# Optimization experiments

Measured on AMD Instinct MI355X. Metric: run time of the kernel, lower is better.

Reference implementation:

```python
import math
import jax, jax.numpy as jnp
import numpy as np

RMS_EPS = 1.1920929e-07  # torch.finfo(float32).eps used by F.rms_norm default

def _rms_norm(x):
    return x * jax.lax.rsqrt(jnp.mean(jnp.square(x), axis=-1, keepdims=True) + RMS_EPS)

def _rope(x, cos, sin):
    # x: [B,T,H,D]; cos/sin: [T, D//2]
    d = x.shape[-1] // 2
    x1, x2 = x[..., :d], x[..., d:]
    c = cos[None, :, None, :]
    s = sin[None, :, None, :]
    return jnp.concatenate([x1 * c + x2 * s, -x1 * s + x2 * c], axis=-1).astype(x.dtype)

def setup_inputs():
    key = jax.random.key(0)
    ks = jax.random.split(key, 8)
    B, T, C, H, D = 2, 2048, 2048, 16, 128
    x = jax.random.normal(ks[0], (B, T, C), dtype=jnp.float32)
    # real RoPE tables for [T, D//2]
    half = D // 2
    inv_freq = 1.0 / (10000.0 ** (np.arange(half, dtype=np.float32) / half))
    ang = np.outer(np.arange(T, dtype=np.float32), inv_freq)
    cos = jnp.asarray(np.cos(ang), dtype=jnp.float32)
    sin = jnp.asarray(np.sin(ang), dtype=jnp.float32)
    s = 0.02
    Wq = jax.random.normal(ks[1], (C, H * D), dtype=jnp.float32) * s
    Wk = jax.random.normal(ks[2], (C, H * D), dtype=jnp.float32) * s
    Wv = jax.random.normal(ks[3], (C, H * D), dtype=jnp.float32) * s
    Wo = jax.random.normal(ks[4], (C, C), dtype=jnp.float32) * s
    fgate_w = jax.random.normal(ks[5], (C, H), dtype=jnp.float32) * s
    fgate_b = jnp.zeros((H,), dtype=jnp.float32)
    weight_lambda = jax.random.normal(ks[6], (C, H), dtype=jnp.float32) * s
    return dict(x=x, cos=cos, sin=sin, Wq=Wq, Wk=Wk, Wv=Wv, Wo=Wo,
                fgate_w=fgate_w, fgate_b=fgate_b, weight_lambda=weight_lambda,
                window_size=1024)

def reference(x, cos, sin, Wq, Wk, Wv, Wo, fgate_w, fgate_b, weight_lambda, window_size):
    B, T, C = x.shape
    H = fgate_w.shape[1]
    D = Wq.shape[1] // H
    sm_scale = 1.0 / math.sqrt(D)
    # QKV projections (bias=False)
    q = (x @ Wq).reshape(B, T, H, D)
    k = (x @ Wk).reshape(B, T, H, D)
    v = (x @ Wv).reshape(B, T, H, D)
    # RoPE then parameter-free RMSNorm on q,k
    q = _rms_norm(_rope(q, cos, sin))
    k = _rms_norm(_rope(k, cos, sin))
    # [B,H,T,D]
    q = q.transpose(0, 2, 1, 3)
    k = k.transpose(0, 2, 1, 3)
    v = v.transpose(0, 2, 1, 3)
    # forgetting gate: log f_t per (B,H,T)
    lam = jax.nn.elu((x @ weight_lambda).astype(jnp.float32)) + 1.0          # [B,T,H]
    logit = (x @ fgate_w + fgate_b) * lam                                    # [B,T,H]
    log_fgate = (jax.nn.log_sigmoid(logit) / (lam + 0.001)).transpose(0, 2, 1)  # [B,H,T]
    cumF = jnp.cumsum(log_fgate, axis=-1)                                    # [B,H,T]
    # forgetting flash attention, dense reference: bias_ij = cumF_i - cumF_j
    scores = jnp.einsum('bhqd,bhkd->bhqk', q.astype(jnp.float32), k.astype(jnp.float32)) * sm_scale
    scores = scores + cumF[..., :, None] - cumF[..., None, :]
    i = jnp.arange(T)[:, None]
    j = jnp.arange(T)[None, :]
    allowed = (j <= i) & (i - j < window_size)  # causal + sliding window
    scores = jnp.where(allowed, scores, -jnp.inf)
    attn = jax.nn.softmax(scores, axis=-1)
    y = jnp.einsum('bhqk,bhkd->bhqd', attn, v.astype(jnp.float32)).astype(x.dtype)
    y = y.transpose(0, 2, 1, 3).reshape(B, T, C)
    return y @ Wo
```

## Files before the change

### kernel.cpp

```cpp
#include <hip/hip_runtime.h>
#include <hip/hip_bf16.h>
#include <stdint.h>

#define T_SEQ 2048
#define CDIM  2048
#define NHEAD 16
#define DHEAD 128
#define BT    4096
#define BHT   32
#define NQKV  6144

typedef __bf16 bf16x8_t __attribute__((ext_vector_type(8)));
typedef float  f32x4_t  __attribute__((ext_vector_type(4)));
typedef unsigned short u16x8_t __attribute__((ext_vector_type(8)));
typedef unsigned short u16x4_t __attribute__((ext_vector_type(4)));

__device__ __forceinline__ unsigned short f2bf(float f){
  unsigned int u = __float_as_uint(f);
  u += 0x7fffu + ((u >> 16) & 1u);
  return (unsigned short)(u >> 16);
}
__device__ __forceinline__ float bf2f(unsigned short h){
  return __uint_as_float(((unsigned int)h) << 16);
}
__device__ __forceinline__ unsigned ldsaddr(const void* p){
  return (unsigned)(size_t)(const __attribute__((address_space(3))) void*)p;
}
__device__ __forceinline__ u16x4_t tr16(unsigned a){
  u16x4_t r;
  asm volatile("ds_read_b64_tr_b16 %0, %1" : "=v"(r) : "v"(a));
  return r;
}

__global__ __launch_bounds__(256) void transpose_cast(const float* __restrict__ W,
                                                      unsigned short* __restrict__ Wt){
  __shared__ float tile[32][33];
  int n0 = blockIdx.x*32, k0 = blockIdx.y*32;
  int tx = threadIdx.x, ty = threadIdx.y;
  #pragma unroll
  for (int i=0;i<32;i+=8)
    tile[ty+i][tx] = W[(size_t)(k0+ty+i)*CDIM + n0 + tx];
  __syncthreads();
  #pragma unroll
  for (int i=0;i<32;i+=8)
    Wt[(size_t)(n0+ty+i)*CDIM + k0 + tx] = f2bf(tile[tx][ty+i]);
}

__global__ __launch_bounds__(256) void build_wgt(const float* __restrict__ fgw,
                                                 const float* __restrict__ wlam,
                                                 float* __restrict__ WgT){
  int idx = blockIdx.x*256 + threadIdx.x;
  int c = idx >> 11, k = idx & 2047;
  const float* W = (c < 16) ? fgw : wlam;
  WgT[idx] = W[k*16 + (c & 15)];
}


#define V3_SYNC() do{ __builtin_amdgcn_sched_barrier(0); \
  __builtin_amdgcn_s_barrier(); \
  asm volatile("s_waitcnt lgkmcnt(0)" ::: "memory"); \
  __builtin_amdgcn_sched_barrier(0); }while(0)

#define V3_TAIL() do{ asm volatile("s_waitcnt vmcnt(3)" ::: "memory"); \
  __builtin_amdgcn_sched_barrier(0); \
  __builtin_amdgcn_s_barrier(); }while(0)

#define V3_MFMA() do{ __builtin_amdgcn_s_setprio(1); \
  _Pragma("unroll") for (int mi=0;mi<4;mi++) \
  _Pragma("unroll") for (int ni=0;ni<4;ni++) \
    acc[mi][ni] = __builtin_amdgcn_mfma_f32_16x16x32_bf16(af[mi], bfr[ni], acc[mi][ni],0,0,0); \
  __builtin_amdgcn_s_setprio(0); }while(0)

#define V3_PHASE(BUF, TIDX) do{ \
  readA(BUF); readB(BUF); \
  { int ts_ = (TIDX)+2; if (ts_ > ntm1) ts_ = ntm1; stage(((BUF)+2)%3, ts_); } \
  V3_SYNC(); V3_MFMA(); V3_TAIL(); }while(0)

template<int MODE>
__global__ __launch_bounds__(512, 2) void gemm_v3(const unsigned short* __restrict__ A,
                                                  const unsigned short* __restrict__ Bt,
                                                  void* __restrict__ Cout,
                                                  int M, int N, int K){
  extern __shared__ unsigned short lds[];
  const int nx = N >> 8;
  const int Mt = M >> 7;
  const int bid = blockIdx.x;
  const int c8 = bid & 7, w = bid >> 3;
  const int mh = Mt >> 1;
  const int mt = (c8 & 1)*mh + (w % mh);
  const int ntc = (c8 >> 1)*(nx >> 2) + (w / mh);
  const int m0 = mt << 7, n0 = ntc << 8;
  const int tid = threadIdx.x, lane = tid & 63, wv = tid >> 6;
  const int wm = wv >> 2, wn = wv & 3;
  const int g = lane >> 4, qi = lane & 15;
  const int ntm1 = (K >> 5) - 1;

  f32x4_t acc[4][4] = {};
  bf16x8_t af[4], bfr[4];

  int goffA, goffB[2];
  { int s = tid; int row = s >> 2; int lg = (s & 3) ^ ((row >> 1) & 3);
    goffA = row*K + lg*8; }
  #pragma unroll
  for (int j=0;j<2;j++){
    int s = j*512 + tid;
    int row = s >> 2;
    int lg = (s & 3) ^ ((row >> 1) & 3);
    goffB[j] = row*K + lg*8;
  }

  auto stage = [&](int buf, int kt){
    const unsigned short* srcA = A + (size_t)m0*K + kt*32;
    const unsigned short* srcB = Bt + (size_t)n0*K + kt*32;
    unsigned short* base = lds + buf*12288;
    __builtin_amdgcn_global_load_lds(
        (const __attribute__((address_space(1))) void*)(srcA + goffA),
        (__attribute__((address_space(3))) void*)(base + tid*8), 16, 0, 0);
    #pragma unroll
    for (int j=0;j<2;j++)
      __builtin_amdgcn_global_load_lds(
        (const __attribute__((address_space(1))) void*)(srcB + goffB[j]),
        (__attribute__((address_space(3))) void*)(base + 4096 + (j*512 + tid)*8), 16, 0, 0);
  };
  auto readA = [&](int buf){
    const unsigned short* base = lds + buf*12288;
    #pragma unroll
    for (int mi=0;mi<4;mi++){
      int row = wm*64 + mi*16 + qi;
      int gs = g ^ ((row >> 1) & 3);
      af[mi] = *reinterpret_cast<const bf16x8_t*>(base + (row*4 + gs)*8);
    }
  };
  auto readB = [&](int buf){
    const unsigned short* base = lds + buf*12288 + 4096;
    #pragma unroll
    for (int ni=0;ni<4;ni++){
      int row = wn*64 + ni*16 + qi;
      int gs = g ^ ((row >> 1) & 3);
      bfr[ni] = *reinterpret_cast<const bf16x8_t*>(base + (row*4 + gs)*8);
    }
  };

  stage(0,0); stage(1,1);
  asm volatile("s_waitcnt vmcnt(3)" ::: "memory");
  __builtin_amdgcn_sched_barrier(0);
  __builtin_amdgcn_s_barrier();

  for (int it=0; it<21; ++it){
    const int t3 = it*3;
    V3_PHASE(0, t3+0);
    V3_PHASE(1, t3+1);
    V3_PHASE(2, t3+2);
  }
  V3_PHASE(0, 63);
  asm volatile("s_waitcnt vmcnt(0)" ::: "memory");

  #pragma unroll
  for (int mi=0;mi<4;mi++){
    #pragma unroll
    for (int ni=0;ni<4;ni++){
      #pragma unroll
      for (int r=0;r<4;r++){
        int mm = m0 + wm*64 + mi*16 + 4*g + r;
        int nn = n0 + wn*64 + ni*16 + qi;
        float v = acc[mi][ni][r];
        if (MODE == 2){
          ((float*)Cout)[(size_t)mm*N + nn] = v;
        } else {
          int bb2 = mm >> 11, t = mm & (T_SEQ-1);
          int which = nn >> 11;
          int hh = (nn >> 7) & 15, d = nn & (DHEAD-1);
          ((unsigned short*)Cout)[(size_t)which*8388608 +
              (((size_t)bb2*NHEAD + hh)*T_SEQ + t)*DHEAD + d] = f2bf(v);
        }
      }
    }
  }
}

#define GROWS 4
__global__ __launch_bounds__(256) void gates_kernel(const float* __restrict__ x,
    const float* __restrict__ WgT, const float* __restrict__ fgb,
    float* __restrict__ lfg, unsigned short* __restrict__ xb){
  __shared__ float xs[GROWS*2048];
  __shared__ float part[GROWS*32*8];
  const int r0 = blockIdx.x*GROWS;
  const int tid = threadIdx.x;
  const float* xp = x + (size_t)r0*CDIM;
  #pragma unroll
  for (int i=0;i<GROWS*2048/(256*4); i++){
    int e = (i*256+tid)*4;
    *(float4*)(xs+e) = *(const float4*)(xp+e);
  }
  __syncthreads();
  #pragma unroll
  for (int i=0;i<GROWS*2048/(256*8); i++){
    int e = (i*256+tid)*8;
    u16x8_t ob;
    #pragma unroll
    for (int j=0;j<8;j++) ob[j] = f2bf(xs[e+j]);
    *reinterpret_cast<u16x8_t*>(xb + (size_t)r0*CDIM + e) = ob;
  }
  const int c = tid & 31, kseg = tid >> 5;
  const float* wp = WgT + c*2048 + kseg*256;
  const float* xq = xs + kseg*256;
  f32x4_t acc[GROWS] = {};
  for (int kk=0; kk<64; kk++){
    f32x4_t wv = *(const f32x4_t*)(wp + kk*4);
    #pragma unroll
    for (int r=0;r<GROWS;r++){
      f32x4_t xv = *(const f32x4_t*)(xq + r*2048 + kk*4);
      acc[r] += xv*wv;
    }
  }
  #pragma unroll
  for (int r=0;r<GROWS;r++)
    part[(r*32 + c)*8 + kseg] = acc[r][0]+acc[r][1]+acc[r][2]+acc[r][3];
  __syncthreads();
  if (tid < GROWS*32){
    const int r = tid >> 5, c2 = tid & 31;
    const float* pp = part + (r*32+c2)*8;
    float s = pp[0]+pp[1]+pp[2]+pp[3]+pp[4]+pp[5]+pp[6]+pp[7];
    float other = __shfl_xor(s, 16, 64);
    if (c2 < 16){
      float df = s, dl = other;
      float lam = (dl > 0.f) ? (dl + 1.f) : __expf(dl);
      float logit = (df + fgb[c2]) * lam;
      float ls = fminf(logit, 0.f) - log1pf(__expf(-fabsf(logit)));
      float lf = ls / (lam + 0.001f);
      int row = r0 + r;
      int b = row >> 11, t = row & (T_SEQ-1);
      lfg[((size_t)b*NHEAD + c2)*T_SEQ + t] = lf;
    }
  }
}

__global__ __launch_bounds__(256) void cumsum_kernel(const float* __restrict__ lfg,
                                                     float* __restrict__ cumF){
  __shared__ float sums[256];
  const int bh = blockIdx.x;
  const float* in = lfg + (size_t)bh*T_SEQ;
  float* out = cumF + (size_t)bh*T_SEQ;
  const int tid = threadIdx.x;
  float4 a = *(const float4*)(in + tid*8);
  float4 b = *(const float4*)(in + tid*8 + 4);
  float v[8] = {a.x,a.y,a.z,a.w,b.x,b.y,b.z,b.w};
  float run = 0.f;
  #pragma unroll
  for (int e=0;e<8;e++) run += v[e];
  sums[tid] = run;
  __syncthreads();
  for (int off=1; off<256; off<<=1){
    float y = (tid >= off) ? sums[tid-off] : 0.f;
    __syncthreads();
    sums[tid] += y;
    __syncthreads();
  }
  float acc = sums[tid] - run;
  float o[8];
  #pragma unroll
  for (int e=0;e<8;e++){ acc += v[e]; o[e] = acc; }
  *(float4*)(out + tid*8)     = make_float4(o[0],o[1],o[2],o[3]);
  *(float4*)(out + tid*8 + 4) = make_float4(o[4],o[5],o[6],o[7]);
}

__global__ __launch_bounds__(256) void rope_rms(unsigned short* __restrict__ QK,
    const float* __restrict__ cosT, const float* __restrict__ sinT){
  const int tid = threadIdx.x, lane = tid & 63, wv = tid >> 6;
  const int idx2 = blockIdx.x*4 + wv;
  const int which = idx2 >> 16;
  const int row = idx2 & 65535;
  const int t = row & (T_SEQ-1);
  unsigned short* xp = QK + (size_t)which*8388608 + (size_t)row*DHEAD;
  float x1 = bf2f(xp[lane]);
  float x2 = bf2f(xp[lane+64]);
  float c = cosT[t*64 + lane];
  float s = sinT[t*64 + lane];
  float o1 = x1*c + x2*s;
  float o2 = x2*c - x1*s;
  float ss = o1*o1 + o2*o2;
  #pragma unroll
  for (int off=1; off<64; off<<=1) ss += __shfl_xor(ss, off, 64);
  float scale = rsqrtf(ss*(1.f/128.f) + 1.1920929e-07f);
  xp[lane]    = f2bf(o1*scale);
  xp[lane+64] = f2bf(o2*scale);
}

__global__ __launch_bounds__(256, 2) void attn_kernel(const unsigned short* __restrict__ Qh,
    const unsigned short* __restrict__ Kh, const unsigned short* __restrict__ Vh,
    const float* __restrict__ cumF, unsigned short* __restrict__ Y,
    const int* __restrict__ winp){
  __shared__ unsigned short smem[32768];
  const int dlin = blockIdx.y*16 + blockIdx.x;
  const int c8 = dlin & 7, klin = dlin >> 3;
  const int bh = c8 + 8*(klin >> 4);
  const int q0b = (klin & 15)*128;
  const int b = bh >> 4, h = bh & 15;
  const int tid = threadIdx.x, lane = tid & 63, wv = tid >> 6;
  const int g = lane >> 4, qi = lane & 15;
  const int win = *winp;
  const unsigned short* Qp = Qh + (size_t)bh*T_SEQ*DHEAD;
  const unsigned short* Kp = Kh + (size_t)bh*T_SEQ*DHEAD;
  const unsigned short* Vp = Vh + (size_t)bh*T_SEQ*DHEAD;
  const float* cF = cumF + (size_t)bh*T_SEQ;
  const int q0w = q0b + wv*32;
  bf16x8_t qf[2][4];
  float cFq[2];
  #pragma unroll
  for (int qb=0;qb<2;qb++){
    cFq[qb] = cF[q0w + qb*16 + qi];
    #pragma unroll
    for (int dt=0;dt<4;dt++)
      qf[qb][dt] = *reinterpret_cast<const bf16x8_t*>(Qp + (size_t)(q0w + qb*16 + qi)*DHEAD + dt*32 + g*8);
  }
  f32x4_t ot[2][8] = {};
  float mrun[2] = {-1e30f, -1e30f}, lrun[2] = {0.f, 0.f};
  const float sm_scale = 0.08838834764831845f;
  int kbeg = q0b - win + 1; if (kbeg < 0) kbeg = 0; kbeg &= ~63;
  const int nt = (q0b + 128 - kbeg) >> 6;

  auto stage = [&](int bi, int k0s){
    unsigned short* Kd = smem + bi*8192;
    unsigned short* Vd = smem + 16384 + bi*8192;
    #pragma unroll
    for (int jj=0;jj<4;jj++){
      int t = (wv*4+jj)*64 + lane;
      int r = t>>4, cc = t&15;
      __builtin_amdgcn_global_load_lds(
        (const __attribute__((address_space(1))) void*)(Kp + (size_t)(k0s+r)*DHEAD + ((cc ^ (r&7))*8)),
        (__attribute__((address_space(3))) void*)(Kd + t*8), 16, 0, 0);
      int dd = t>>7, kq = (t>>3)&15, rr = (t>>1)&3, hb = t&1;
      __builtin_amdgcn_global_load_lds(
        (const __attribute__((address_space(1))) void*)(Vp + (size_t)(k0s + kq*4 + rr)*DHEAD + dd*16 + hb*8),
        (__attribute__((address_space(3))) void*)(Vd + t*8), 16, 0, 0);
    }
  };

  stage(0, kbeg);
  for (int it=0; it<nt; ++it){
    const int k0 = kbeg + it*64;
    const int cur = it & 1;
    __syncthreads();
    if (it+1 < nt) stage(cur^1, k0+64);
    if (k0 <= q0w+31 && (k0 + 63) >= (q0w - win + 1)){
      const unsigned short* Kc = smem + cur*8192;
      f32x4_t s[2][4] = {};
      __builtin_amdgcn_s_setprio(1);
      #pragma unroll
      for (int dt=0;dt<4;dt++){
        bf16x8_t kf[4];
        #pragma unroll
        for (int kb=0;kb<4;kb++){
          int row = kb*16 + qi;
          kf[kb] = *reinterpret_cast<const bf16x8_t*>(Kc + row*128 + (((dt*4+g) ^ (row&7))*8));
        }
        #pragma unroll
        for (int kb=0;kb<4;kb++){
          s[0][kb] = __builtin_amdgcn_mfma_f32_16x16x32_bf16(kf[kb], qf[0][dt], s[0][kb], 0,0,0);
          s[1][kb] = __builtin_amdgcn_mfma_f32_16x16x32_bf16(kf[kb], qf[1][dt], s[1][kb], 0,0,0);
        }
      }
      __builtin_amdgcn_s_setprio(0);
      float4 cb[4];
      #pragma unroll
      for (int kb=0;kb<4;kb++) cb[kb] = *(const float4*)(cF + k0 + kb*16 + 4*g);
      u16x8_t pb[2][2];
      #pragma unroll
      for (int qb=0;qb<2;qb++){
        const int qg = q0w + qb*16 + qi;
        float p[16], tmax = -INFINITY;
        #pragma unroll
        for (int kb=0;kb<4;kb++){
          #pragma unroll
          for (int r=0;r<4;r++){
            int key = k0 + kb*16 + 4*g + r;
            float sv = fmaf(s[qb][kb][r], sm_scale, cFq[qb] - ((const float*)&cb[kb])[r]);
            bool ok = (key <= qg) && (qg - key < win);
            p[kb*4+r] = ok ? sv : -INFINITY;
            tmax = fmaxf(tmax, p[kb*4+r]);
          }
        }
        tmax = fmaxf(tmax, __shfl_xor(tmax, 16, 64));
        tmax = fmaxf(tmax, __shfl_xor(tmax, 32, 64));
        float mnew = fmaxf(mrun[qb], tmax);
        float alpha = __expf(mrun[qb] - mnew);
        float tsum = 0.f;
        #pragma unroll
        for (int i2=0;i2<16;i2++){ p[i2] = __expf(p[i2] - mnew); tsum += p[i2]; }
        tsum += __shfl_xor(tsum, 16, 64);
        tsum += __shfl_xor(tsum, 32, 64);
        lrun[qb] = lrun[qb]*alpha + tsum;
        mrun[qb] = mnew;
        #pragma unroll
        for (int dt=0;dt<8;dt++) ot[qb][dt] *= alpha;
        #pragma unroll
        for (int cc=0;cc<2;cc++){
          #pragma unroll
          for (int e=0;e<8;e++)
            pb[qb][cc][e] = f2bf(p[(2*cc + (e>>2))*4 + (e&3)]);
        }
      }
      unsigned vbase = ldsaddr(smem + 16384 + cur*8192) + lane*8;
      #pragma unroll
      for (int cc=0;cc<2;cc++){
        u16x4_t vlo[8], vhi[8];
        #pragma unroll
        for (int dt=0;dt<8;dt++){
          vlo[dt] = tr16(vbase + (unsigned)((dt*16 + 8*cc)*128));
          vhi[dt] = tr16(vbase + (unsigned)((dt*16 + 8*cc + 4)*128));
        }
        asm volatile("s_waitcnt lgkmcnt(0)");
        __builtin_amdgcn_sched_barrier(0);
        __builtin_amdgcn_s_setprio(1);
        #pragma unroll
        for (int dt=0;dt<8;dt++){
          u16x8_t vv = __builtin_shufflevector(vlo[dt], vhi[dt], 0,1,2,3,4,5,6,7);
          bf16x8_t vf = *reinterpret_cast<bf16x8_t*>(&vv);
          ot[0][dt] = __builtin_amdgcn_mfma_f32_16x16x32_bf16(vf, *reinterpret_cast<bf16x8_t*>(&pb[0][cc]), ot[0][dt], 0,0,0);
          ot[1][dt] = __builtin_amdgcn_mfma_f32_16x16x32_bf16(vf, *reinterpret_cast<bf16x8_t*>(&pb[1][cc]), ot[1][dt], 0,0,0);
        }
        __builtin_amdgcn_s_setprio(0);
      }
    }
  }
  __syncthreads();
  float invl[2] = {1.f/lrun[0], 1.f/lrun[1]};
  #pragma unroll
  for (int qb=0;qb<2;qb++){
    int qlocal = wv*32 + qb*16 + qi;
    #pragma unroll
    for (int dt=0;dt<8;dt++){
      int d8 = dt*2 + (g>>1);
      u16x4_t w;
      #pragma unroll
      for (int r=0;r<4;r++) w[r] = f2bf(ot[qb][dt][r]*invl[qb]);
      *reinterpret_cast<u16x4_t*>(smem + qlocal*128 + ((d8 ^ (qlocal&7))*8) + 4*(g&1)) = w;
    }
  }
  __syncthreads();
  #pragma unroll
  for (int i=0;i<8;i++){
    int t = i*256 + tid;
    int row = t>>4, cc = t&15;
    u16x8_t v = *reinterpret_cast<const u16x8_t*>(smem + row*128 + ((cc ^ (row&7))*8));
    *reinterpret_cast<u16x8_t*>(Y + ((size_t)b*T_SEQ + q0b + row)*CDIM + h*DHEAD + cc*8) = v;
  }
}

extern "C" void kernel_launch(void* const* d_in, const int* in_sizes, int n_in,
                              void* d_out, int out_size, void* d_ws, size_t ws_size,
                              hipStream_t stream){
  const float* x    = (const float*)d_in[0];
  const float* cosT = (const float*)d_in[1];
  const float* sinT = (const float*)d_in[2];
  const float* Wq   = (const float*)d_in[3];
  const float* Wk   = (const float*)d_in[4];
  const float* Wv   = (const float*)d_in[5];
  const float* Wo   = (const float*)d_in[6];
  const float* fgw  = (const float*)d_in[7];
  const float* fgb  = (const float*)d_in[8];
  const float* wlam = (const float*)d_in[9];
  const int*   winp = (const int*)d_in[10];

  char* ws = (char*)d_ws;
  unsigned short* xb    = (unsigned short*)(ws + 0);
  unsigned short* WqkvT = (unsigned short*)(ws + 16777216);
  unsigned short* WoT   = (unsigned short*)(ws + 41943040);
  unsigned short* QKVh  = (unsigned short*)(ws + 50331648);
  unsigned short* Qh = QKVh;
  unsigned short* Kh = QKVh + 8388608;
  unsigned short* Vh = QKVh + 16777216;
  unsigned short* Yb  = (unsigned short*)(ws + 100663296);
  float* lfg  = (float*)(ws + 117440512);
  float* cumF = (float*)(ws + 117702656);
  float* WgT  = (float*)(ws + 117964800);

  build_wgt<<<256, 256, 0, stream>>>(fgw, wlam, WgT);
  gates_kernel<<<BT/GROWS, 256, 0, stream>>>(x, WgT, fgb, lfg, xb);
  cumsum_kernel<<<BHT, 256, 0, stream>>>(lfg, cumF);

  dim3 tgrid(64,64), tblk(32,8);
  transpose_cast<<<tgrid, tblk, 0, stream>>>(Wq, WqkvT);
  transpose_cast<<<tgrid, tblk, 0, stream>>>(Wk, WqkvT + 4194304);
  transpose_cast<<<tgrid, tblk, 0, stream>>>(Wv, WqkvT + 8388608);
  transpose_cast<<<tgrid, tblk, 0, stream>>>(Wo, WoT);

  hipFuncSetAttribute(reinterpret_cast<const void*>(&gemm_v3<1>),
      hipFuncAttributeMaxDynamicSharedMemorySize, 73728);
  hipFuncSetAttribute(reinterpret_cast<const void*>(&gemm_v3<2>),
      hipFuncAttributeMaxDynamicSharedMemorySize, 73728);

  gemm_v3<1><<<(BT/128)*(NQKV/256), 512, 73728, stream>>>(xb, WqkvT, QKVh, BT, NQKV, CDIM);

  rope_rms<<<2*BHT*T_SEQ/4, 256, 0, stream>>>(QKVh, cosT, sinT);

  attn_kernel<<<dim3(16, BHT), 256, 0, stream>>>(Qh, Kh, Vh, cumF, Yb, winp);

  gemm_v3<2><<<(BT/128)*(CDIM/256), 512, 73728, stream>>>(Yb, WoT, d_out, BT, CDIM, CDIM);
}
```

Before: 290.2 us.

## Add 128x128 output-projection GEMM and streamline attention softmax with exp2 and masking skip

Swaps the output-projection GEMM for a new 128x128-tile kernel with a triple-buffered 32-wide K pipeline. It launches twice as many blocks with two blocks per CU, aiming at better occupancy for the small N=2048 GEMM. In attention, cumF and the softmax scale are pre-multiplied by log2(e) so exp2 can be used, the mask is skipped for interior tiles, and the running max is rescaled only when some lane's max grows. Probabilities are packed with v_cvt_pk_bf16_f32. These changes raise risks of register pressure and a rounding-mode difference in the bf16 packing.

```diff
diff --git a/kernel.cpp b/kernel.cpp
--- a/kernel.cpp
+++ b/kernel.cpp
@@ -9,11 +9,13 @@
 #define BT    4096
 #define BHT   32
 #define NQKV  6144
+#define LOG2E 1.4426950408889634f
 
 typedef __bf16 bf16x8_t __attribute__((ext_vector_type(8)));
 typedef float  f32x4_t  __attribute__((ext_vector_type(4)));
 typedef unsigned short u16x8_t __attribute__((ext_vector_type(8)));
 typedef unsigned short u16x4_t __attribute__((ext_vector_type(4)));
+typedef unsigned int   u32x4_t __attribute__((ext_vector_type(4)));
 
 __device__ __forceinline__ unsigned short f2bf(float f){
   unsigned int u = __float_as_uint(f);
@@ -178,6 +180,106 @@
   }
 }
 
+
+#define W_SYNC() V3_SYNC()
+#define W_TAIL() do{ asm volatile("s_waitcnt vmcnt(2)" ::: "memory"); \
+  __builtin_amdgcn_sched_barrier(0); \
+  __builtin_amdgcn_s_barrier(); }while(0)
+
+#define W_MFMA() do{ __builtin_amdgcn_s_setprio(1); \
+  _Pragma("unroll") for (int mi=0;mi<4;mi++) \
+  _Pragma("unroll") for (int ni=0;ni<2;ni++) \
+    acc[mi][ni] = __builtin_amdgcn_mfma_f32_16x16x32_bf16(af[mi], bfr[ni], acc[mi][ni],0,0,0); \
+  __builtin_amdgcn_s_setprio(0); }while(0)
+
+#define W_PHASE(BUF, TIDX) do{ \
+  readA(BUF); readB(BUF); \
+  { int ts_ = (TIDX)+2; if (ts_ > ntm1) ts_ = ntm1; stage(((BUF)+2)%3, ts_); } \
+  W_SYNC(); W_MFMA(); W_TAIL(); }while(0)
+
+__global__ __launch_bounds__(512, 2) void gemm_w(const unsigned short* __restrict__ A,
+                                                 const unsigned short* __restrict__ Bt,
+                                                 float* __restrict__ Cout,
+                                                 int M, int N, int K){
+  extern __shared__ unsigned short lds[];
+  const int nx = N >> 7;
+  const int Mt = M >> 7;
+  const int bid = blockIdx.x;
+  const int c8 = bid & 7, w = bid >> 3;
+  const int mh = Mt >> 1;
+  const int mt = (c8 & 1)*mh + (w % mh);
+  const int ntc = (c8 >> 1)*(nx >> 2) + (w / mh);
+  const int m0 = mt << 7, n0 = ntc << 7;
+  const int tid = threadIdx.x, lane = tid & 63, wv = tid >> 6;
+  const int wm = wv >> 2, wn = wv & 3;
+  const int g = lane >> 4, qi = lane & 15;
+  const int ntm1 = (K >> 5) - 1;
+
+  f32x4_t acc[4][2] = {};
+  bf16x8_t af[4], bfr[2];
+
+  int goff;
+  { int s = tid; int row = s >> 2; int lg = (s & 3) ^ ((row >> 1) & 3);
+    goff = row*K + lg*8; }
+
+  auto stage = [&](int buf, int kt){
+    const unsigned short* srcA = A + (size_t)m0*K + kt*32;
+    const unsigned short* srcB = Bt + (size_t)n0*K + kt*32;
+    unsigned short* base = lds + buf*8192;
+    __builtin_amdgcn_global_load_lds(
+        (const __attribute__((address_space(1))) void*)(srcA + goff),
+        (__attribute__((address_space(3))) void*)(base + tid*8), 16, 0, 0);
+    __builtin_amdgcn_global_load_lds(
+        (const __attribute__((address_space(1))) void*)(srcB + goff),
+        (__attribute__((address_space(3))) void*)(base + 4096 + tid*8), 16, 0, 0);
+  };
+  auto readA = [&](int buf){
+    const unsigned short* base = lds + buf*8192;
+    #pragma unroll
+    for (int mi=0;mi<4;mi++){
+      int row = wm*64 + mi*16 + qi;
+      int gs = g ^ ((row >> 1) & 3);
+      af[mi] = *reinterpret_cast<const bf16x8_t*>(base + (row*4 + gs)*8);
+    }
+  };
+  auto readB = [&](int buf){
+    const unsigned short* base = lds + buf*8192 + 4096;
+    #pragma unroll
+    for (int ni=0;ni<2;ni++){
+      int row = wn*32 + ni*16 + qi;
+      int gs = g ^ ((row >> 1) & 3);
+      bfr[ni] = *reinterpret_cast<const bf16x8_t*>(base + (row*4 + gs)*8);
+    }
+  };
+
+  stage(0,0); stage(1,1);
+  asm volatile("s_waitcnt vmcnt(2)" ::: "memory");
+  __builtin_amdgcn_sched_barrier(0);
+  __builtin_amdgcn_s_barrier();
+
+  for (int it=0; it<21; ++it){
+    const int t3 = it*3;
+    W_PHASE(0, t3+0);
+    W_PHASE(1, t3+1);
+    W_PHASE(2, t3+2);
+  }
+  W_PHASE(0, 63);
+  asm volatile("s_waitcnt vmcnt(0)" ::: "memory");
+
+  #pragma unroll
+  for (int mi=0;mi<4;mi++){
+    #pragma unroll
+    for (int ni=0;ni<2;ni++){
+      #pragma unroll
+      for (int r=0;r<4;r++){
+        int mm = m0 + wm*64 + mi*16 + 4*g + r;
+        int nn = n0 + wn*32 + ni*16 + qi;
+        Cout[(size_t)mm*N + nn] = acc[mi][ni][r];
+      }
+    }
+  }
+}
+
 #define GROWS 4
 __global__ __launch_bounds__(256) void gates_kernel(const float* __restrict__ x,
     const float* __restrict__ WgT, const float* __restrict__ fgb,
@@ -259,7 +361,7 @@
   float acc = sums[tid] - run;
   float o[8];
   #pragma unroll
-  for (int e=0;e<8;e++){ acc += v[e]; o[e] = acc; }
+  for (int e=0;e<8;e++){ acc += v[e]; o[e] = acc*LOG2E; }
   *(float4*)(out + tid*8)     = make_float4(o[0],o[1],o[2],o[3]);
   *(float4*)(out + tid*8 + 4) = make_float4(o[4],o[5],o[6],o[7]);
 }
@@ -315,7 +417,7 @@
   }
   f32x4_t ot[2][8] = {};
   float mrun[2] = {-1e30f, -1e30f}, lrun[2] = {0.f, 0.f};
-  const float sm_scale = 0.08838834764831845f;
+  const float sm2 = 0.08838834764831845f * LOG2E;
   int kbeg = q0b - win + 1; if (kbeg < 0) kbeg = 0; kbeg &= ~63;
   const int nt = (q0b + 128 - kbeg) >> 6;
 
@@ -364,40 +466,60 @@
       float4 cb[4];
       #pragma unroll
       for (int kb=0;kb<4;kb++) cb[kb] = *(const float4*)(cF + k0 + kb*16 + 4*g);
-      u16x8_t pb[2][2];
+      const bool interior = (k0 + 63 <= q0w) && (k0 >= q0w + 32 - win);
+      u32x4_t pbw[2][2];
       #pragma unroll
       for (int qb=0;qb<2;qb++){
         const int qg = q0w + qb*16 + qi;
         float p[16], tmax = -INFINITY;
-        #pragma unroll
-        for (int kb=0;kb<4;kb++){
+        if (interior){
           #pragma unroll
-          for (int r=0;r<4;r++){
-            int key = k0 + kb*16 + 4*g + r;
-            float sv = fmaf(s[qb][kb][r], sm_scale, cFq[qb] - ((const float*)&cb[kb])[r]);
-            bool ok = (key <= qg) && (qg - key < win);
-            p[kb*4+r] = ok ? sv : -INFINITY;
-            tmax = fmaxf(tmax, p[kb*4+r]);
+          for (int kb=0;kb<4;kb++){
+            #pragma unroll
+            for (int r=0;r<4;r++){
+              float sv = fmaf(s[qb][kb][r], sm2, cFq[qb] - ((const float*)&cb[kb])[r]);
+              p[kb*4+r] = sv;
+              tmax = fmaxf(tmax, sv);
+            }
+          }
+        } else {
+          #pragma unroll
+          for (int kb=0;kb<4;kb++){
+            #pragma unroll
+            for (int r=0;r<4;r++){
+              int key = k0 + kb*16 + 4*g + r;
+              float sv = fmaf(s[qb][kb][r], sm2, cFq[qb] - ((const float*)&cb[kb])[r]);
+              bool ok = (key <= qg) && (qg - key < win);
+              p[kb*4+r] = ok ? sv : -INFINITY;
+              tmax = fmaxf(tmax, p[kb*4+r]);
+            }
           }
         }
         tmax = fmaxf(tmax, __shfl_xor(tmax, 16, 64));
         tmax = fmaxf(tmax, __shfl_xor(tmax, 32, 64));
-        float mnew = fmaxf(mrun[qb], tmax);
-        float alpha = __expf(mrun[qb] - mnew);
+        if (__any(tmax > mrun[qb])){
+          float mnew = fmaxf(mrun[qb], tmax);
+          float alpha = exp2f(mrun[qb] - mnew);
+          lrun[qb] *= alpha;
+          #pragma unroll
+          for (int dt=0;dt<8;dt++) ot[qb][dt] *= alpha;
+          mrun[qb] = mnew;
+        }
         float tsum = 0.f;
         #pragma unroll
-        for (int i2=0;i2<16;i2++){ p[i2] = __expf(p[i2] - mnew); tsum += p[i2]; }
+        for (int i2=0;i2<16;i2++){ p[i2] = exp2f(p[i2] - mrun[qb]); tsum += p[i2]; }
         tsum += __shfl_xor(tsum, 16, 64);
         tsum += __shfl_xor(tsum, 32, 64);
-        lrun[qb] = lrun[qb]*alpha + tsum;
-        mrun[qb] = mnew;
-        #pragma unroll
-        for (int dt=0;dt<8;dt++) ot[qb][dt] *= alpha;
+        lrun[qb] += tsum;
         #pragma unroll
         for (int cc=0;cc<2;cc++){
           #pragma unroll
-          for (int e=0;e<8;e++)
-            pb[qb][cc][e] = f2bf(p[(2*cc + (e>>2))*4 + (e&3)]);
+          for (int j=0;j<4;j++){
+            unsigned wpk;
+            asm("v_cvt_pk_bf16_f32 %0, %1, %2" : "=v"(wpk)
+                : "v"(p[8*cc+2*j]), "v"(p[8*cc+2*j+1]));
+            pbw[qb][cc][j] = wpk;
+          }
         }
       }
       unsigned vbase = ldsaddr(smem + 16384 + cur*8192) + lane*8;
@@ -416,8 +538,8 @@
         for (int dt=0;dt<8;dt++){
           u16x8_t vv = __builtin_shufflevector(vlo[dt], vhi[dt], 0,1,2,3,4,5,6,7);
           bf16x8_t vf = *reinterpret_cast<bf16x8_t*>(&vv);
-          ot[0][dt] = __builtin_amdgcn_mfma_f32_16x16x32_bf16(vf, *reinterpret_cast<bf16x8_t*>(&pb[0][cc]), ot[0][dt], 0,0,0);
-          ot[1][dt] = __builtin_amdgcn_mfma_f32_16x16x32_bf16(vf, *reinterpret_cast<bf16x8_t*>(&pb[1][cc]), ot[1][dt], 0,0,0);
+          ot[0][dt] = __builtin_amdgcn_mfma_f32_16x16x32_bf16(vf, *reinterpret_cast<bf16x8_t*>(&pbw[0][cc]), ot[0][dt], 0,0,0);
+          ot[1][dt] = __builtin_amdgcn_mfma_f32_16x16x32_bf16(vf, *reinterpret_cast<bf16x8_t*>(&pbw[1][cc]), ot[1][dt], 0,0,0);
         }
         __builtin_amdgcn_s_setprio(0);
       }
@@ -487,8 +609,8 @@
 
   hipFuncSetAttribute(reinterpret_cast<const void*>(&gemm_v3<1>),
       hipFuncAttributeMaxDynamicSharedMemorySize, 73728);
-  hipFuncSetAttribute(reinterpret_cast<const void*>(&gemm_v3<2>),
-      hipFuncAttributeMaxDynamicSharedMemorySize, 73728);
+  hipFuncSetAttribute(reinterpret_cast<const void*>(&gemm_w),
+      hipFuncAttributeMaxDynamicSharedMemorySize, 49152);
 
   gemm_v3<1><<<(BT/128)*(NQKV/256), 512, 73728, stream>>>(xb, WqkvT, QKVh, BT, NQKV, CDIM);
 
@@ -496,5 +618,5 @@
 
   attn_kernel<<<dim3(16, BHT), 256, 0, stream>>>(Qh, Kh, Vh, cumF, Yb, winp);
 
-  gemm_v3<2><<<(BT/128)*(CDIM/256), 512, 73728, stream>>>(Yb, WoT, d_out, BT, CDIM, CDIM);
-}
+  gemm_w<<<(BT/128)*(CDIM/128), 512, 49152, stream>>>(Yb, WoT, (float*)d_out, BT, CDIM, CDIM);
+}
```

Measured after the change: 298.1 us. 2.7% more time.
